# Performance work log

Hardware: AMD Instinct MI355X
Metric: run time of the kernel (lower is better)

Reference implementation:

```python
import jax, jax.numpy as jnp
import numpy as np


def setup_inputs() -> dict:
    key = jax.random.key(0)
    inputs = jax.random.normal(key, (8, 2048, 512), dtype=jnp.float32)
    return {"inputs": inputs}


def reference(inputs) -> jnp.ndarray:
    # score[b,i,j] = <x_i, x_j>  (no 1/sqrt(d) scaling in the original)
    score = jnp.einsum("bsd,btd->bst", inputs, inputs)  # [B,S,S]
    distribution = jax.nn.softmax(score, axis=-1)
    # output = distribution @ inputs
    return jnp.einsum("bst,btd->bsd", distribution, inputs)
```

## Files before the change

### kernel.cpp

```cpp
#include <hip/hip_runtime.h>
#include <hip/hip_bf16.h>

#define BATCH 8
#define SEQ   2048
#define DIM   512
#define QB    32
#define KB    64
#define NT    512
#define NKV   (SEQ / KB)

typedef __attribute__((ext_vector_type(8))) short short8;
typedef __attribute__((ext_vector_type(4))) float f32x4;
typedef __attribute__((ext_vector_type(4))) unsigned short ushort4v;

__device__ __forceinline__ unsigned short f2bf(float f) {
    union { float f; unsigned u; } v; v.f = f;
    return (unsigned short)((v.u + 0x7FFFu + ((v.u >> 16) & 1u)) >> 16);
}

__device__ __forceinline__ int swz(int kv) {
    return (8 * (kv & 7)) ^ (16 * ((kv >> 3) & 3)) ^ (64 * ((kv >> 3) & 1));
}

__global__ __launch_bounds__(256)
void prep_kernel(const float* __restrict__ X,
                 unsigned short* __restrict__ Xbf,
                 unsigned short* __restrict__ Xt) {
    __shared__ unsigned short T[64][72];
    const int b  = blockIdx.z;
    const int s0 = blockIdx.x * 64;
    const int d0 = blockIdx.y * 64;
    const int tid = threadIdx.x;
    const float* Xb = X + ((size_t)b * SEQ + s0) * DIM + d0;
    unsigned short* Yb = Xbf + ((size_t)b * SEQ + s0) * DIM + d0;
    #pragma unroll
    for (int r = 0; r < 4; ++r) {
        const int s = (tid >> 4) + r * 16;
        const int d = (tid & 15) * 4;
        float4 v = *(const float4*)(Xb + (size_t)s * DIM + d);
        ushort4v h;
        h[0] = f2bf(v.x); h[1] = f2bf(v.y); h[2] = f2bf(v.z); h[3] = f2bf(v.w);
        *(ushort4v*)(Yb + (size_t)s * DIM + d) = h;
        *(ushort4v*)&T[s][d] = h;
    }
    __syncthreads();
    {
        const int d = tid >> 2;
        const int sc = (tid & 3) * 16;
        unsigned short buf[16];
        #pragma unroll
        for (int j = 0; j < 16; ++j) buf[j] = T[sc + j][d];
        unsigned short* o = Xt + ((size_t)b * DIM + d0 + d) * SEQ + s0 + sc;
        *(short8*)(o)     = *(short8*)&buf[0];
        *(short8*)(o + 8) = *(short8*)&buf[8];
    }
}

__device__ __forceinline__ void stage_K(const unsigned short* __restrict__ Xb,
                                        unsigned short* klds, int t, int w, int lane) {
    const unsigned short* kp = Xb + (size_t)(t * KB) * DIM;
    #pragma unroll
    for (int k = 0; k < 8; ++k) {
        const int kv = k * 8 + w;
        const int dsrc = (lane * 8) ^ swz(kv);
        const unsigned short* g = kp + (size_t)kv * DIM + dsrc;
        unsigned short* l = klds + kv * DIM;
        __builtin_amdgcn_global_load_lds(
            (__attribute__((address_space(1))) void*)(g),
            (__attribute__((address_space(3))) void*)(l), 16, 0, 0);
    }
}

__device__ __forceinline__ void stage_V(const unsigned short* __restrict__ Xtb,
                                        unsigned short* vtlds, int t, int w, int lane) {
    #pragma unroll
    for (int k = 0; k < 8; ++k) {
        const int r = w * 64 + k * 8 + (lane >> 3);
        const int kvsrc = ((lane & 7) * 8) ^ (8 * (r & 7));
        const unsigned short* g = Xtb + (size_t)r * SEQ + t * KB + kvsrc;
        unsigned short* l = vtlds + (w * 64 + k * 8) * KB;
        __builtin_amdgcn_global_load_lds(
            (__attribute__((address_space(1))) void*)(g),
            (__attribute__((address_space(3))) void*)(l), 16, 0, 0);
    }
}

__global__ __launch_bounds__(NT, 2)
void attn_fwd(const unsigned short* __restrict__ Xbf,
              const unsigned short* __restrict__ Xt,
              float* __restrict__ O) {
    const int b   = blockIdx.x & 7;
    const int qt  = blockIdx.x >> 3;
    const int tid = threadIdx.x;
    const int lane = tid & 63;
    const int w    = tid >> 6;
    const int col  = lane & 15;
    const int kgrp = lane >> 4;

    __shared__ alignas(16) unsigned short Klds[KB * DIM];
    __shared__ alignas(16) unsigned short Vtlds[DIM * KB];
    __shared__ alignas(16) float Sbuf[QB][KB + 4];
    __shared__ alignas(16) unsigned short Pfrag[2][2][64][8];
    __shared__ float m_s[QB], l_s[QB], fac_s[QB];

    const unsigned short* Xb  = Xbf + (size_t)b * SEQ * DIM;
    const unsigned short* Xtb = Xt  + (size_t)b * DIM * SEQ;

    const int qs = w >> 2;
    const int kc = w & 3;
    short8 qfrag[16];
    {
        const int qrow = qt * QB + qs * 16 + col;
        const unsigned short* qp = Xb + (size_t)qrow * DIM;
        #pragma unroll
        for (int ks = 0; ks < 16; ++ks)
            qfrag[ks] = *(const short8*)(qp + ks * 32 + kgrp * 8);
    }

    if (tid < QB) { m_s[tid] = -INFINITY; l_s[tid] = 0.f; }

    f32x4 oacc[2][4];
    #pragma unroll
    for (int i = 0; i < 2; ++i)
        #pragma unroll
        for (int j = 0; j < 4; ++j)
            oacc[i][j] = (f32x4){0.f, 0.f, 0.f, 0.f};

    for (int t = 0; t < NKV; ++t) {
        stage_K(Xb,  Klds,  t, w, lane);
        stage_V(Xtb, Vtlds, t, w, lane);
        asm volatile("s_waitcnt vmcnt(0)" ::: "memory");
        __syncthreads();

        {
            const int kvrow = kc * 16 + col;
            const unsigned short* kbase = &Klds[kvrow * DIM];
            const int sw = swz(kvrow);
            f32x4 sacc = (f32x4){0.f,0.f,0.f,0.f};
            #pragma unroll
            for (int ks = 0; ks < 16; ++ks) {
                short8 kfr = *(const short8*)(kbase + ((ks * 32 + kgrp * 8) ^ sw));
                sacc = __builtin_amdgcn_mfma_f32_16x16x32_bf16(qfrag[ks], kfr, sacc, 0, 0, 0);
            }
            #pragma unroll
            for (int r = 0; r < 4; ++r)
                Sbuf[qs * 16 + kgrp * 4 + r][kc * 16 + col] = sacc[r];
        }
        __syncthreads();

        {
            const int r = tid >> 4;
            const int c = tid & 15;
            float4 sa = *(const float4*)&Sbuf[r][c * 4];
            float mloc = fmaxf(fmaxf(sa.x, sa.y), fmaxf(sa.z, sa.w));
            mloc = fmaxf(mloc, __shfl_xor(mloc, 1));
            mloc = fmaxf(mloc, __shfl_xor(mloc, 2));
            mloc = fmaxf(mloc, __shfl_xor(mloc, 4));
            mloc = fmaxf(mloc, __shfl_xor(mloc, 8));
            const float mold = m_s[r];
            const float mnew = fmaxf(mold, mloc);
            const float fac  = __expf(mold - mnew);
            float p0 = __expf(sa.x - mnew), p1 = __expf(sa.y - mnew);
            float p2 = __expf(sa.z - mnew), p3 = __expf(sa.w - mnew);
            float lsum = (p0 + p1) + (p2 + p3);
            lsum += __shfl_xor(lsum, 1);
            lsum += __shfl_xor(lsum, 2);
            lsum += __shfl_xor(lsum, 4);
            lsum += __shfl_xor(lsum, 8);
            ushort4v p4;
            p4[0] = f2bf(p0); p4[1] = f2bf(p1); p4[2] = f2bf(p2); p4[3] = f2bf(p3);
            *(ushort4v*)&Pfrag[r >> 4][c >> 3][(r & 15) + 16 * ((c >> 1) & 3)][(c & 1) * 4] = p4;
            if (c == 0) {
                m_s[r] = mnew;
                fac_s[r] = fac;
                l_s[r] = l_s[r] * fac + lsum;
            }
        }
        __syncthreads();

        #pragma unroll
        for (int q2 = 0; q2 < 2; ++q2) {
            #pragma unroll
            for (int r = 0; r < 4; ++r) {
                const float f = fac_s[q2 * 16 + kgrp * 4 + r];
                #pragma unroll
                for (int dt = 0; dt < 4; ++dt) oacc[q2][dt][r] *= f;
            }
        }
        #pragma unroll
        for (int kc2 = 0; kc2 < 2; ++kc2) {
            const int kvb = kc2 * 32 + kgrp * 8;
            short8 afr[2];
            #pragma unroll
            for (int q2 = 0; q2 < 2; ++q2)
                afr[q2] = *(const short8*)&Pfrag[q2][kc2][lane][0];
            #pragma unroll
            for (int dt = 0; dt < 4; ++dt) {
                const int d = w * 64 + dt * 16 + col;
                const short8 bfr = *(const short8*)&Vtlds[d * KB + (kvb ^ (8 * (d & 7)))];
                #pragma unroll
                for (int q2 = 0; q2 < 2; ++q2)
                    oacc[q2][dt] = __builtin_amdgcn_mfma_f32_16x16x32_bf16(afr[q2], bfr, oacc[q2][dt], 0, 0, 0);
            }
        }
        __syncthreads();
    }

    #pragma unroll
    for (int q2 = 0; q2 < 2; ++q2) {
        #pragma unroll
        for (int r = 0; r < 4; ++r) {
            const int row = q2 * 16 + kgrp * 4 + r;
            const float inv = 1.f / l_s[row];
            float* op = O + ((size_t)b * SEQ + qt * QB + row) * DIM + w * 64 + col;
            #pragma unroll
            for (int dt = 0; dt < 4; ++dt)
                op[dt * 16] = oacc[q2][dt][r] * inv;
        }
    }
}

extern "C" void kernel_launch(void* const* d_in, const int* in_sizes, int n_in,
                              void* d_out, int out_size, void* d_ws, size_t ws_size,
                              hipStream_t stream) {
    const float* X = (const float*)d_in[0];
    float* Out = (float*)d_out;
    unsigned short* Xbf = (unsigned short*)d_ws;
    unsigned short* Xt  = Xbf + (size_t)BATCH * SEQ * DIM;

    dim3 pgrid(SEQ / 64, DIM / 64, BATCH);
    hipLaunchKernelGGL(prep_kernel, pgrid, dim3(256), 0, stream, X, Xbf, Xt);

    dim3 grid(BATCH * (SEQ / QB));
    dim3 block(NT);
    hipLaunchKernelGGL(attn_fwd, grid, block, 0, stream, Xbf, Xt, Out);
}
```

Before: 200.6 us.

## Load K fragments directly from global and double-buffer V tiles in LDS

Result: slower. 372.7 us (+85.8%).

```diff
diff --git a/kernel.cpp b/kernel.cpp
--- a/kernel.cpp
+++ b/kernel.cpp
@@ -16,10 +16,6 @@
 __device__ __forceinline__ unsigned short f2bf(float f) {
     union { float f; unsigned u; } v; v.f = f;
     return (unsigned short)((v.u + 0x7FFFu + ((v.u >> 16) & 1u)) >> 16);
-}
-
-__device__ __forceinline__ int swz(int kv) {
-    return (8 * (kv & 7)) ^ (16 * ((kv >> 3) & 3)) ^ (64 * ((kv >> 3) & 1));
 }
 
 __global__ __launch_bounds__(256)
@@ -56,21 +52,6 @@
     }
 }
 
-__device__ __forceinline__ void stage_K(const unsigned short* __restrict__ Xb,
-                                        unsigned short* klds, int t, int w, int lane) {
-    const unsigned short* kp = Xb + (size_t)(t * KB) * DIM;
-    #pragma unroll
-    for (int k = 0; k < 8; ++k) {
-        const int kv = k * 8 + w;
-        const int dsrc = (lane * 8) ^ swz(kv);
-        const unsigned short* g = kp + (size_t)kv * DIM + dsrc;
-        unsigned short* l = klds + kv * DIM;
-        __builtin_amdgcn_global_load_lds(
-            (__attribute__((address_space(1))) void*)(g),
-            (__attribute__((address_space(3))) void*)(l), 16, 0, 0);
-    }
-}
-
 __device__ __forceinline__ void stage_V(const unsigned short* __restrict__ Xtb,
                                         unsigned short* vtlds, int t, int w, int lane) {
     #pragma unroll
@@ -97,8 +78,7 @@
     const int col  = lane & 15;
     const int kgrp = lane >> 4;
 
-    __shared__ alignas(16) unsigned short Klds[KB * DIM];
-    __shared__ alignas(16) unsigned short Vtlds[DIM * KB];
+    __shared__ alignas(16) unsigned short Vtlds[2][DIM * KB];
     __shared__ alignas(16) float Sbuf[QB][KB + 4];
     __shared__ alignas(16) unsigned short Pfrag[2][2][64][8];
     __shared__ float m_s[QB], l_s[QB], fac_s[QB];
@@ -126,20 +106,20 @@
         for (int j = 0; j < 4; ++j)
             oacc[i][j] = (f32x4){0.f, 0.f, 0.f, 0.f};
 
+    stage_V(Xtb, &Vtlds[0][0], 0, w, lane);
+    asm volatile("s_waitcnt vmcnt(0)" ::: "memory");
+    __syncthreads();
+
     for (int t = 0; t < NKV; ++t) {
-        stage_K(Xb,  Klds,  t, w, lane);
-        stage_V(Xtb, Vtlds, t, w, lane);
-        asm volatile("s_waitcnt vmcnt(0)" ::: "memory");
-        __syncthreads();
+        const int cur = t & 1;
+        if (t + 1 < NKV) stage_V(Xtb, &Vtlds[cur ^ 1][0], t + 1, w, lane);
 
         {
-            const int kvrow = kc * 16 + col;
-            const unsigned short* kbase = &Klds[kvrow * DIM];
-            const int sw = swz(kvrow);
+            const unsigned short* krow = Xb + (size_t)(t * KB + kc * 16 + col) * DIM;
             f32x4 sacc = (f32x4){0.f,0.f,0.f,0.f};
             #pragma unroll
             for (int ks = 0; ks < 16; ++ks) {
-                short8 kfr = *(const short8*)(kbase + ((ks * 32 + kgrp * 8) ^ sw));
+                short8 kfr = *(const short8*)(krow + ks * 32 + kgrp * 8);
                 sacc = __builtin_amdgcn_mfma_f32_16x16x32_bf16(qfrag[ks], kfr, sacc, 0, 0, 0);
             }
             #pragma unroll
@@ -197,12 +177,14 @@
             #pragma unroll
             for (int dt = 0; dt < 4; ++dt) {
                 const int d = w * 64 + dt * 16 + col;
-                const short8 bfr = *(const short8*)&Vtlds[d * KB + (kvb ^ (8 * (d & 7)))];
+                const short8 bfr = *(const short8*)&Vtlds[cur][d * KB + (kvb ^ (8 * (d & 7)))];
                 #pragma unroll
                 for (int q2 = 0; q2 < 2; ++q2)
                     oacc[q2][dt] = __builtin_amdgcn_mfma_f32_16x16x32_bf16(afr[q2], bfr, oacc[q2][dt], 0, 0, 0);
             }
         }
+
+        asm volatile("s_waitcnt vmcnt(0)" ::: "memory");
         __syncthreads();
     }
 
```
